# Performance work log

Hardware: AMD Instinct MI355X
Metric: run time of the kernel (lower is better)

The kernel has to match this reference:

```python
import jax, jax.numpy as jnp
import numpy as np

B, V = 1024, 4096
CHUNK = 16  # rows of x per cdist chunk; bounds intermediate to CHUNK*B*V floats (~268MB)
T = 2.0      # module hardcodes self.T = 2 regardless of init arg
EPS = 0.1
N_ITERS = 20


def _cdist_l1(x, y):
    # torch.cdist(x, y, p=1): out[i, j] = sum_v |x[i, v] - y[j, v]| -> [B, B]
    # chunk over rows of x to avoid materializing [B, B, V]
    xc = x.reshape(B // CHUNK, CHUNK, V)
    f = lambda xb: jnp.sum(jnp.abs(xb[:, None, :] - y[None, :, :]), axis=-1)  # [CHUNK, B]
    return jax.lax.map(f, xc).reshape(B, B)


def setup_inputs() -> dict:
    key = jax.random.key(0)
    k1, k2 = jax.random.split(key)
    y_s = jax.random.normal(k1, (B, V), dtype=jnp.float32)
    y_t = jax.random.normal(k2, (B, V), dtype=jnp.float32)
    return {"y_s": y_s, "y_t": y_t}


def reference(y_s, y_t):
    p_s = jax.nn.softmax(y_s / T, axis=1)
    p_t = jax.nn.softmax(y_t / T, axis=1)
    Wxy = _cdist_l1(p_s, p_t)          # [B, B] L1 cost matrix
    K = jnp.exp(-Wxy / EPS)

    def body(P, _):
        P = P / jnp.sum(P, axis=1, keepdims=True)  # row normalize
        P = P / jnp.sum(P, axis=0, keepdims=True)  # col normalize
        return P, None

    P, _ = jax.lax.scan(body, K, None, length=N_ITERS)
    return 0.001 * jnp.sum(P * Wxy)
```

## Files before the change

### kernel.cpp

```cpp
#include <hip/hip_runtime.h>
#include <hip/hip_fp16.h>

#define BSZ 1024
#define VSZ 4096
#define NBLK 32
#define JPB 32
#define KPAD 1040

__global__ __launch_bounds__(256) void softmax_kernel(const float* __restrict__ ys,
                                                      const float* __restrict__ yt,
                                                      unsigned short* __restrict__ ps,
                                                      unsigned short* __restrict__ pt) {
    int row = blockIdx.x;
    const float* src;
    unsigned short* dst;
    if (row < BSZ) { src = ys + (size_t)row * VSZ;         dst = ps + (size_t)row * VSZ; }
    else           { src = yt + (size_t)(row - BSZ) * VSZ; dst = pt + (size_t)(row - BSZ) * VSZ; }
    int t = threadIdx.x;
    float4 v[4];
    float m = -1e30f;
#pragma unroll
    for (int k = 0; k < 4; ++k) {
        v[k] = ((const float4*)src)[t + 256 * k];
        m = fmaxf(m, fmaxf(fmaxf(v[k].x, v[k].y), fmaxf(v[k].z, v[k].w)));
    }
#pragma unroll
    for (int d = 32; d >= 1; d >>= 1) m = fmaxf(m, __shfl_down(m, d));
    __shared__ float sred[4];
    __shared__ float sred2[4];
    int lane = t & 63, wid = t >> 6;
    if (lane == 0) sred[wid] = m;
    __syncthreads();
    m = fmaxf(fmaxf(sred[0], sred[1]), fmaxf(sred[2], sred[3]));
    const float C = 0.7213475204444817f;
    float s = 0.f;
#pragma unroll
    for (int k = 0; k < 4; ++k) {
        v[k].x = exp2f((v[k].x - m) * C);
        v[k].y = exp2f((v[k].y - m) * C);
        v[k].z = exp2f((v[k].z - m) * C);
        v[k].w = exp2f((v[k].w - m) * C);
        s += (v[k].x + v[k].y) + (v[k].z + v[k].w);
    }
#pragma unroll
    for (int d = 32; d >= 1; d >>= 1) s += __shfl_down(s, d);
    if (lane == 0) sred2[wid] = s;
    __syncthreads();
    s = (sred2[0] + sred2[1]) + (sred2[2] + sred2[3]);
    float inv = 65535.0f / s;
#pragma unroll
    for (int k = 0; k < 4; ++k) {
        union { unsigned short h[4]; uint2 u; } o;
        o.h[0] = (unsigned short)__float2uint_rn(fminf(v[k].x * inv, 65535.0f));
        o.h[1] = (unsigned short)__float2uint_rn(fminf(v[k].y * inv, 65535.0f));
        o.h[2] = (unsigned short)__float2uint_rn(fminf(v[k].z * inv, 65535.0f));
        o.h[3] = (unsigned short)__float2uint_rn(fminf(v[k].w * inv, 65535.0f));
        ((uint2*)dst)[t + 256 * k] = o.u;
    }
}

#define TSI 128
#define TSJ 64
#define LSTR 72

__global__ __launch_bounds__(256, 1) void cdist_kernel(const unsigned short* __restrict__ psh,
                                                       const unsigned short* __restrict__ pth,
                                                       float* __restrict__ spart) {
    __shared__ unsigned short sP[2][TSI * LSTR];
    __shared__ unsigned short sQ[2][TSJ * LSTR];
    const int bi = blockIdx.x;
    const int bj = blockIdx.y;
    const int bv = blockIdx.z;
    const int t = threadIdx.x;
    const int cl = t & 15;
    const int rl = t >> 4;

    const int pr = t >> 1, pc = (t & 1) * 32;
    const int qr = t >> 2, qc = (t & 3) * 16;
    const unsigned short* gP = psh + (size_t)(bi * TSI + pr) * VSZ + bv * 1024 + pc;
    const unsigned short* gQ = pth + (size_t)(bj * TSJ + qr) * VSZ + bv * 1024 + qc;
    unsigned short* lP0 = &sP[0][pr * LSTR + pc];
    unsigned short* lQ0 = &sQ[0][qr * LSTR + qc];

    unsigned acc[4][8];
#pragma unroll
    for (int w = 0; w < 4; ++w)
#pragma unroll
        for (int u = 0; u < 8; ++u) acc[w][u] = 0u;

    {
        uint4 a0 = *(const uint4*)(gP + 0);
        uint4 a1 = *(const uint4*)(gP + 8);
        uint4 a2 = *(const uint4*)(gP + 16);
        uint4 a3 = *(const uint4*)(gP + 24);
        uint4 b0 = *(const uint4*)(gQ + 0);
        uint4 b1 = *(const uint4*)(gQ + 8);
        *(uint4*)(lP0 + 0)  = a0;
        *(uint4*)(lP0 + 8)  = a1;
        *(uint4*)(lP0 + 16) = a2;
        *(uint4*)(lP0 + 24) = a3;
        *(uint4*)(lQ0 + 0)  = b0;
        *(uint4*)(lQ0 + 8)  = b1;
    }
    __syncthreads();

    for (int kt = 0; kt < 16; ++kt) {
        const int cb = kt & 1;
        uint4 rp0, rp1, rp2, rp3, rq0, rq1;
        if (kt < 15) {
            const unsigned short* gp = gP + (kt + 1) * 64;
            const unsigned short* gq = gQ + (kt + 1) * 64;
            rp0 = *(const uint4*)(gp + 0);
            rp1 = *(const uint4*)(gp + 8);
            rp2 = *(const uint4*)(gp + 16);
            rp3 = *(const uint4*)(gp + 24);
            rq0 = *(const uint4*)(gq + 0);
            rq1 = *(const uint4*)(gq + 8);
        }
        const unsigned short* pbase = sP[cb] + cl * LSTR;
        const unsigned short* qbase = sQ[cb] + rl * LSTR;
#pragma unroll
        for (int vv = 0; vv < 8; ++vv) {
            uint4 q[4];
#pragma unroll
            for (int w = 0; w < 4; ++w)
                q[w] = *(const uint4*)(qbase + w * 16 * LSTR + vv * 8);
#pragma unroll
            for (int h = 0; h < 4; ++h) {
                uint4 p0 = *(const uint4*)(pbase + (2 * h + 0) * 16 * LSTR + vv * 8);
                uint4 p1 = *(const uint4*)(pbase + (2 * h + 1) * 16 * LSTR + vv * 8);
#pragma unroll
                for (int w = 0; w < 4; ++w) {
                    unsigned a = acc[w][2 * h + 0];
                    a = __builtin_amdgcn_sad_u16(p0.x, q[w].x, a);
                    a = __builtin_amdgcn_sad_u16(p0.y, q[w].y, a);
                    a = __builtin_amdgcn_sad_u16(p0.z, q[w].z, a);
                    a = __builtin_amdgcn_sad_u16(p0.w, q[w].w, a);
                    acc[w][2 * h + 0] = a;
                    unsigned b = acc[w][2 * h + 1];
                    b = __builtin_amdgcn_sad_u16(p1.x, q[w].x, b);
                    b = __builtin_amdgcn_sad_u16(p1.y, q[w].y, b);
                    b = __builtin_amdgcn_sad_u16(p1.z, q[w].z, b);
                    b = __builtin_amdgcn_sad_u16(p1.w, q[w].w, b);
                    acc[w][2 * h + 1] = b;
                }
            }
        }
        if (kt < 15) {
            unsigned short* lp = lP0 + (cb ^ 1) * (TSI * LSTR);
            unsigned short* lq = lQ0 + (cb ^ 1) * (TSJ * LSTR);
            *(uint4*)(lp + 0)  = rp0;
            *(uint4*)(lp + 8)  = rp1;
            *(uint4*)(lp + 16) = rp2;
            *(uint4*)(lp + 24) = rp3;
            *(uint4*)(lq + 0)  = rq0;
            *(uint4*)(lq + 8)  = rq1;
            __syncthreads();
        }
    }

    float* outp = spart + (size_t)bv * (BSZ * BSZ);
    const float SCL = 1.0f / 65535.0f;
#pragma unroll
    for (int w = 0; w < 4; ++w) {
        size_t jr = (size_t)(bj * TSJ + rl + 16 * w);
#pragma unroll
        for (int u = 0; u < 8; ++u) {
            int ic = bi * TSI + cl + 16 * u;
            outp[jr * BSZ + ic] = (float)acc[w][u] * SCL;
        }
    }
}

__global__ __launch_bounds__(256) void combine_kernel(const float* __restrict__ spart,
                                                      float* __restrict__ wt,
                                                      float* __restrict__ kt,
                                                      float* __restrict__ cpart,
                                                      unsigned* __restrict__ flags) {
    if (blockIdx.x == 0 && threadIdx.x < NBLK) flags[threadIdx.x * 32] = 0u;
    if (blockIdx.x < 3) {
        float4 z4; z4.x = z4.y = z4.z = z4.w = 0.f;
        ((float4*)cpart)[blockIdx.x * 256 + threadIdx.x] = z4;
    }
    int idx = blockIdx.x * 256 + threadIdx.x;
    const float4* p0 = (const float4*)spart;
    const int Q = (BSZ * BSZ) / 4;
    float4 a = p0[idx], b = p0[idx + Q], c = p0[idx + 2 * Q], d = p0[idx + 3 * Q];
    float4 w;
    w.x = (a.x + b.x) + (c.x + d.x);
    w.y = (a.y + b.y) + (c.y + d.y);
    w.z = (a.z + b.z) + (c.z + d.z);
    w.w = (a.w + b.w) + (c.w + d.w);
    ((float4*)wt)[idx] = w;
    const float CE = -14.426950408889634f;
    float4 k;
    k.x = exp2f(w.x * CE);
    k.y = exp2f(w.y * CE);
    k.z = exp2f(w.z * CE);
    k.w = exp2f(w.w * CE);
    ((float4*)kt)[idx] = k;
}

__device__ inline void grid_barrier(unsigned* flags, unsigned gen) {
    __syncthreads();
    const int t = threadIdx.x;
    if (t == 0)
        __hip_atomic_store(&flags[blockIdx.x * 32], gen, __ATOMIC_RELEASE, __HIP_MEMORY_SCOPE_AGENT);
    if (t < NBLK) {
        while (__hip_atomic_load(&flags[t * 32], __ATOMIC_RELAXED, __HIP_MEMORY_SCOPE_AGENT) < gen)
            __builtin_amdgcn_s_sleep(1);
    }
    __syncthreads();
    if (t == 0)
        (void)__hip_atomic_load(&flags[0], __ATOMIC_ACQUIRE, __HIP_MEMORY_SCOPE_AGENT);
    __syncthreads();
}

__global__ __launch_bounds__(512) void sinkhorn_kernel(const float* __restrict__ KT,
                                                       const float* __restrict__ WT,
                                                       float* __restrict__ cpart,
                                                       float* __restrict__ outpart,
                                                       float* __restrict__ out,
                                                       unsigned* __restrict__ flags) {
    __shared__ __align__(16) float k_lds[JPB * KPAD];
    __shared__ __align__(16) float a_sh[BSZ];
    __shared__ float b_sh[JPB];
    __shared__ float red[JPB];
    const int z = blockIdx.x;
    const int t = threadIdx.x;
    const int j0 = z * JPB;
#pragma unroll
    for (int m = 0; m < 16; ++m) {
        int idx = t + 512 * m;
        int row = idx >> 8;
        int col = (idx & 255) * 4;
        float4 v = *(const float4*)(KT + (size_t)(j0 + row) * BSZ + col);
        *(float4*)(&k_lds[row * KPAD + col]) = v;
    }
    if (t < JPB) b_sh[t] = 1.0f;
    __syncthreads();
    const int jj = t >> 4;
    const int il = t & 15;
    unsigned gen = 1u;
    for (int it = 0; it < 20; ++it) {
        float* cbuf = cpart + (size_t)(it % 3) * BSZ;
        float2 s = {0.f, 0.f};
#pragma unroll
        for (int q = 0; q < JPB; ++q) {
            float2 kv = *(const float2*)(&k_lds[q * KPAD + 2 * t]);
            float bb = b_sh[q];
            s.x += kv.x * bb; s.y += kv.y * bb;
        }
        (void)__hip_atomic_fetch_add(&cbuf[2 * t],     s.x, __ATOMIC_RELAXED, __HIP_MEMORY_SCOPE_AGENT);
        (void)__hip_atomic_fetch_add(&cbuf[2 * t + 1], s.y, __ATOMIC_RELAXED, __HIP_MEMORY_SCOPE_AGENT);
        grid_barrier(flags, gen++);
        float2 cv = *(const float2*)(&cbuf[2 * t]);
        if (t < 32) cpart[(size_t)((it + 2) % 3) * BSZ + z * 32 + t] = 0.f;
        float2 ar;
        ar.x = 1.0f / cv.x; ar.y = 1.0f / cv.y;
        ((float2*)a_sh)[t] = ar;
        __syncthreads();
        float sb = 0.f;
#pragma unroll
        for (int m2 = 0; m2 < 16; ++m2) {
            float4 kv = *(const float4*)(&k_lds[jj * KPAD + (il + 16 * m2) * 4]);
            float4 av = ((const float4*)a_sh)[il + 16 * m2];
            sb += (kv.x * av.x + kv.y * av.y) + (kv.z * av.z + kv.w * av.w);
        }
#pragma unroll
        for (int d = 8; d >= 1; d >>= 1) sb += __shfl_down(sb, d, 16);
        if (il == 0) b_sh[jj] = 1.0f / sb;
        __syncthreads();
    }
    {
        const float4* wrow = (const float4*)(WT + (size_t)(j0 + jj) * BSZ);
        float sb = 0.f;
#pragma unroll 4
        for (int m2 = 0; m2 < 16; ++m2) {
            float4 kv = *(const float4*)(&k_lds[jj * KPAD + (il + 16 * m2) * 4]);
            float4 wv = wrow[il + 16 * m2];
            float4 av = ((const float4*)a_sh)[il + 16 * m2];
            sb += (av.x * kv.x * wv.x + av.y * kv.y * wv.y) +
                  (av.z * kv.z * wv.z + av.w * kv.w * wv.w);
        }
#pragma unroll
        for (int d = 8; d >= 1; d >>= 1) sb += __shfl_down(sb, d, 16);
        if (il == 0) red[jj] = sb * b_sh[jj];
        __syncthreads();
        if (t == 0) {
            float ss = 0.f;
#pragma unroll
            for (int q = 0; q < JPB; ++q) ss += red[q];
            outpart[z] = ss;
        }
    }
    grid_barrier(flags, gen++);
    if (z == 0 && t == 0) {
        float ss = 0.f;
        for (int q = 0; q < NBLK; ++q) ss += outpart[q];
        out[0] = 0.001f * ss;
    }
}

extern "C" void kernel_launch(void* const* d_in, const int* in_sizes, int n_in,
                              void* d_out, int out_size, void* d_ws, size_t ws_size,
                              hipStream_t stream) {
    const float* ys = (const float*)d_in[0];
    const float* yt = (const float*)d_in[1];
    float* ws = (float*)d_ws;
    unsigned short* psh = (unsigned short*)ws;
    unsigned short* pth = (unsigned short*)(ws + 2ull * 1024 * 1024);
    float* spart   = ws + 4ull * 1024 * 1024;
    float* wt      = spart + 4ull * BSZ * BSZ;
    float* kt      = wt + (size_t)BSZ * BSZ;
    float* cpart   = kt + (size_t)BSZ * BSZ;
    float* outpart = cpart + 2ull * NBLK * BSZ;
    unsigned* flags = (unsigned*)(outpart + 128);
    float* outp    = (float*)d_out;

    softmax_kernel<<<dim3(2 * BSZ), dim3(256), 0, stream>>>(ys, yt, psh, pth);
    cdist_kernel<<<dim3(8, 16, 4), dim3(256), 0, stream>>>(psh, pth, spart);
    combine_kernel<<<dim3((BSZ * BSZ / 4) / 256), dim3(256), 0, stream>>>(spart, wt, kt, cpart, flags);

    void* args[] = {(void*)&kt, (void*)&wt, (void*)&cpart, (void*)&outpart, (void*)&outp,
                    (void*)&flags};
    (void)hipLaunchCooperativeKernel((void*)sinkhorn_kernel, dim3(NBLK), dim3(512), args, 0, stream);
}
```

Measured before the change: 317.2 us.

## Drop LDS double buffering in cdist kernel and raise occupancy hint

Replaces the register-prefetched, double-buffered LDS pipeline in the L1 cdist kernel with a single LDS buffer loaded each k-step between two barriers. The launch bound changes from 1 to 4 blocks per CU, which halves LDS use and frees the prefetch registers so more waves can run at once. The aim is to hide global-load latency through occupancy rather than software pipelining. The cost is an extra barrier per iteration and loads that are no longer overlapped within a block.

After: 284.8 us. 1.11x faster.

```diff
diff --git a/kernel.cpp b/kernel.cpp
--- a/kernel.cpp
+++ b/kernel.cpp
@@ -63,11 +63,11 @@
 #define TSJ 64
 #define LSTR 72
 
-__global__ __launch_bounds__(256, 1) void cdist_kernel(const unsigned short* __restrict__ psh,
+__global__ __launch_bounds__(256, 4) void cdist_kernel(const unsigned short* __restrict__ psh,
                                                        const unsigned short* __restrict__ pth,
                                                        float* __restrict__ spart) {
-    __shared__ unsigned short sP[2][TSI * LSTR];
-    __shared__ unsigned short sQ[2][TSJ * LSTR];
+    __shared__ unsigned short sP[TSI * LSTR];
+    __shared__ unsigned short sQ[TSJ * LSTR];
     const int bi = blockIdx.x;
     const int bj = blockIdx.y;
     const int bv = blockIdx.z;
@@ -79,8 +79,8 @@
     const int qr = t >> 2, qc = (t & 3) * 16;
     const unsigned short* gP = psh + (size_t)(bi * TSI + pr) * VSZ + bv * 1024 + pc;
     const unsigned short* gQ = pth + (size_t)(bj * TSJ + qr) * VSZ + bv * 1024 + qc;
-    unsigned short* lP0 = &sP[0][pr * LSTR + pc];
-    unsigned short* lQ0 = &sQ[0][qr * LSTR + qc];
+    unsigned short* lP = &sP[pr * LSTR + pc];
+    unsigned short* lQ = &sQ[qr * LSTR + qc];
 
     unsigned acc[4][8];
 #pragma unroll
@@ -88,37 +88,25 @@
 #pragma unroll
         for (int u = 0; u < 8; ++u) acc[w][u] = 0u;
 
-    {
-        uint4 a0 = *(const uint4*)(gP + 0);
-        uint4 a1 = *(const uint4*)(gP + 8);
-        uint4 a2 = *(const uint4*)(gP + 16);
-        uint4 a3 = *(const uint4*)(gP + 24);
-        uint4 b0 = *(const uint4*)(gQ + 0);
-        uint4 b1 = *(const uint4*)(gQ + 8);
-        *(uint4*)(lP0 + 0)  = a0;
-        *(uint4*)(lP0 + 8)  = a1;
-        *(uint4*)(lP0 + 16) = a2;
-        *(uint4*)(lP0 + 24) = a3;
-        *(uint4*)(lQ0 + 0)  = b0;
-        *(uint4*)(lQ0 + 8)  = b1;
-    }
-    __syncthreads();
-
     for (int kt = 0; kt < 16; ++kt) {
-        const int cb = kt & 1;
-        uint4 rp0, rp1, rp2, rp3, rq0, rq1;
-        if (kt < 15) {
-            const unsigned short* gp = gP + (kt + 1) * 64;
-            const unsigned short* gq = gQ + (kt + 1) * 64;
-            rp0 = *(const uint4*)(gp + 0);
-            rp1 = *(const uint4*)(gp + 8);
-            rp2 = *(const uint4*)(gp + 16);
-            rp3 = *(const uint4*)(gp + 24);
-            rq0 = *(const uint4*)(gq + 0);
-            rq1 = *(const uint4*)(gq + 8);
-        }
-        const unsigned short* pbase = sP[cb] + cl * LSTR;
-        const unsigned short* qbase = sQ[cb] + rl * LSTR;
+        const unsigned short* gp = gP + kt * 64;
+        const unsigned short* gq = gQ + kt * 64;
+        uint4 a0 = *(const uint4*)(gp + 0);
+        uint4 a1 = *(const uint4*)(gp + 8);
+        uint4 a2 = *(const uint4*)(gp + 16);
+        uint4 a3 = *(const uint4*)(gp + 24);
+        uint4 b0 = *(const uint4*)(gq + 0);
+        uint4 b1 = *(const uint4*)(gq + 8);
+        __syncthreads();
+        *(uint4*)(lP + 0)  = a0;
+        *(uint4*)(lP + 8)  = a1;
+        *(uint4*)(lP + 16) = a2;
+        *(uint4*)(lP + 24) = a3;
+        *(uint4*)(lQ + 0)  = b0;
+        *(uint4*)(lQ + 8)  = b1;
+        __syncthreads();
+        const unsigned short* pbase = sP + cl * LSTR;
+        const unsigned short* qbase = sQ + rl * LSTR;
 #pragma unroll
         for (int vv = 0; vv < 8; ++vv) {
             uint4 q[4];
@@ -145,17 +133,6 @@
                     acc[w][2 * h + 1] = b;
                 }
             }
-        }
-        if (kt < 15) {
-            unsigned short* lp = lP0 + (cb ^ 1) * (TSI * LSTR);
-            unsigned short* lq = lQ0 + (cb ^ 1) * (TSJ * LSTR);
-            *(uint4*)(lp + 0)  = rp0;
-            *(uint4*)(lp + 8)  = rp1;
-            *(uint4*)(lp + 16) = rp2;
-            *(uint4*)(lp + 24) = rp3;
-            *(uint4*)(lq + 0)  = rq0;
-            *(uint4*)(lq + 8)  = rq1;
-            __syncthreads();
         }
     }
 
```
